# Performance work log

Measured on AMD Instinct MI355X. Metric: run time of the kernel, lower is better.

## Reference

```python
import jax, jax.numpy as jnp
import numpy as np

WS = 32          # window_size (== k passed to rounding helper)
R = 4            # num_relations
H = 8            # num_heads
D = 64           # out_features (head dim)
FIN = 256        # in_features
LENGTHS = [251, 247, 263, 255, 240, 258, 249, 260, 252, 245, 256, 250, 248, 261, 244, 254]


def _statics(lengths, ws):
    """Static index bookkeeping mirroring round_up_to_nearest_k_and_a_window_size,
    insert_zero_rows and the post-hoc index removal in forward()."""
    l = np.asarray(lengths, dtype=np.int64)
    tgt = (l + ws - 1) // ws * ws + ws            # per-graph padded length (+1 extra window)
    starts = np.concatenate([[0], np.cumsum(tgt)[:-1]])
    pad_even = starts - np.arange(len(l)) * ws + l  # padding start in trimmed frame
    pad_odd_win = (starts + tgt - ws) // ws         # window index of each extra padding window
    L = int(tgt.sum())
    w = L // ws
    # positions of real nodes inside the padded sequence
    pos = np.concatenate([s + np.arange(n) for s, n in zip(starts, l)])
    extra = set(pad_odd_win.tolist())
    rem_windows = np.array([i for i in range(w) if i not in extra], dtype=np.int64)
    Wp = len(rem_windows)
    removed = set()
    for p in pad_even:
        nm = (int(p) + ws - 1) // ws * ws
        removed.update(range(int(p), nm))
    rem_final = np.array([i for i in range(Wp * ws) if i not in removed], dtype=np.int64)
    return L, w, pos, rem_windows, rem_final


def setup_inputs() -> dict:
    key = jax.random.key(0)
    k1, k2, k3, k4, k5 = jax.random.split(key, 5)
    N = int(sum(LENGTHS))
    node_features = jax.random.normal(k1, (R, N, FIN), dtype=jnp.float32)
    Wq = jax.random.normal(k2, (H * D, FIN), dtype=jnp.float32) * 0.02
    b_q = jax.random.normal(k3, (H * D,), dtype=jnp.float32) * 0.02
    Wk = jax.random.normal(k4, (H * D, FIN), dtype=jnp.float32) * 0.02
    b_k = jax.random.normal(k5, (H * D,), dtype=jnp.float32) * 0.02
    num_nodes = jnp.asarray(LENGTHS, dtype=jnp.int64)
    return {"node_features": node_features, "Wq": Wq, "b_q": b_q, "Wk": Wk, "b_k": b_k,
            "num_nodes": num_nodes}


def reference(node_features, Wq, b_q, Wk, b_k, num_nodes):
    lengths = np.asarray(num_nodes).tolist()
    L, w, pos, rem_w, rem_f = _statics(lengths, WS)
    Rr, N, Fi = node_features.shape

    # insert_zero_rows: scatter real nodes into padded [R, L, F]; bool key mask [L]
    padded = jnp.zeros((Rr, L, Fi), node_features.dtype).at[:, pos].set(node_features)
    maskL = np.zeros(L, dtype=bool)
    maskL[pos] = True

    # Q/K projections -> [R*H, L, D]
    Q = (padded @ Wq.T + b_q).reshape(Rr, L, H, D).transpose(0, 2, 1, 3).reshape(Rr * H, L, D)
    K = (padded @ Wk.T + b_k).reshape(Rr, L, H, D).transpose(0, 2, 1, 3).reshape(Rr * H, L, D)

    scale = D ** -0.5
    qb = Q.reshape(-1, w, WS, D) * scale            # [B, w, ws, D]
    kb = K.reshape(-1, w, WS, D)
    # look_around keys (backward=1, forward=1, pad_value=-1)
    pk = jnp.pad(kb, ((0, 0), (1, 1), (0, 0), (0, 0)), constant_values=-1.0)
    k3 = jnp.concatenate([pk[:, i:i + w] for i in range(3)], axis=2)  # [B, w, 3ws, D]

    # static validity mask: key-position pad mask AND look-around of real-node mask
    t = np.arange(L).reshape(w, WS)
    pt = np.pad(t, ((1, 1), (0, 0)), constant_values=-1)
    t3 = np.concatenate([pt[i:i + w] for i in range(3)], axis=1)      # [w, 3ws]
    mw = maskL.reshape(w, WS)
    pm = np.pad(mw, ((1, 1), (0, 0)), constant_values=False)
    m3 = np.concatenate([pm[i:i + w] for i in range(3)], axis=1)      # [w, 3ws]
    valid = jnp.asarray(m3 & (t3 != -1))[None, :, None, :]            # [1, w, 1, 3ws]

    sim = jnp.einsum('bwid,bwjd->bwij', qb, k3)                        # [B, w, ws, 3ws]
    NEG = -jnp.finfo(sim.dtype).max
    sim = jnp.where(valid, sim, NEG)

    # drop pure-padding extra windows, softmax (dropout omitted: eval mode)
    attn = jax.nn.softmax(sim[:, rem_w], axis=-1)                      # [B, Wp, ws, 3ws]
    Wp = rem_w.shape[0]
    score = attn.reshape(Rr, H, Wp, WS, 3 * WS).mean(axis=1)           # [R, Wp, ws, 3ws]

    # displace blocks to banded rectangle, then trim first/last window of columns
    wi = np.arange(Wp)[:, None, None]
    ri = np.arange(WS)[None, :, None]
    ci = (np.arange(Wp) * WS)[:, None, None] + np.arange(3 * WS)[None, None, :]
    full = jnp.zeros((Rr, Wp, WS, (Wp + 2) * WS), score.dtype)
    full = full.at[:, wi, ri, ci].set(score)
    rect = full.reshape(Rr, Wp * WS, (Wp + 2) * WS)[:, :, WS:-WS]      # [R, Wp*ws, Wp*ws]

    # remove intra-window padding rows and columns
    rect = rect[:, rem_f][:, :, rem_f]                                 # [R, N, N]
    n = rem_f.shape[0]
    return rect.transpose(1, 0, 2).reshape(n, Rr * n)                  # [N, R*N]
```

## Files before the change

kernel.cpp:

```cpp
#include <hip/hip_runtime.h>
#include <stdint.h>

typedef float f32x4 __attribute__((ext_vector_type(4)));
typedef short s16x8 __attribute__((ext_vector_type(8)));
typedef unsigned short u16x4 __attribute__((ext_vector_type(4)));
typedef unsigned short u16x8 __attribute__((ext_vector_type(8)));

#define NG 16
__constant__ int c_LEN[NG]   = {251,247,263,255,240,258,249,260,252,245,256,250,248,261,244,254};
__constant__ int c_CUM[NG+1] = {0,251,498,761,1016,1256,1514,1763,2023,2275,2520,2776,3026,3274,3535,3779,4033};
__constant__ int c_KWC[NG+1] = {0,8,16,25,33,41,50,58,67,75,83,91,99,107,116,124,132};

#define NTOT 4033
#define RN   16132
#define NWIN 132
#define NEGF (-3.0e38f)

#define OUT_F32 65060356L
#define OUT_N4  16265089L
#define ZBLOCKS 2024
#define PBLOCKS 4048

#define OFF_WB 8259584
#define OFF_QK 8783872

__device__ __forceinline__ unsigned short f2bf(float f){
  union { float f; uint32_t u; } x; x.f = f;
  uint32_t u = x.u;
  u += 0x7fffu + ((u >> 16) & 1u);
  return (unsigned short)(u >> 16);
}

__device__ __forceinline__ f32x4 mfma16(s16x8 a, s16x8 b, f32x4 c){
  return __builtin_amdgcn_mfma_f32_16x16x32_bf16(a, b, c, 0, 0, 0);
}

#define NX4  1032448
#define NWQ4 32768
#define NCV4 1097984
__global__ void convert_kernel(const float* __restrict__ X,
                               const float* __restrict__ Wq,
                               const float* __restrict__ Wk,
                               unsigned short* __restrict__ Xb,
                               unsigned short* __restrict__ Wb){
  int i = blockIdx.x * 256 + threadIdx.x;
  if (i >= NCV4) return;
  const float* src; unsigned short* dst;
  if (i < NX4){ src = X + (size_t)i * 4; dst = Xb + (size_t)i * 4; }
  else {
    int k = i - NX4;
    if (k < NWQ4){ src = Wq + (size_t)k * 4; dst = Wb + (size_t)k * 4; }
    else         { src = Wk + (size_t)(k - NWQ4) * 4; dst = Wb + (size_t)k * 4; }
  }
  f32x4 v = *(const f32x4*)src;
  u16x4 o;
  #pragma unroll
  for (int c = 0; c < 4; ++c) o[c] = f2bf(v[c]);
  *(u16x4*)dst = o;
}

#define LP 68
__global__ __launch_bounds__(256) void projzero_kernel(const unsigned short* __restrict__ Xb,
                                                       const unsigned short* __restrict__ Wb,
                                                       const float* __restrict__ bq,
                                                       const float* __restrict__ bk,
                                                       unsigned short* __restrict__ QK,
                                                       float* __restrict__ out){
  __shared__ float tile[64 * LP];

  int bid = blockIdx.x;
  int grp = bid / 3;
  int rem = bid - grp * 3;

  if (rem == 2){
    f32x4 z = {0.f, 0.f, 0.f, 0.f};
    f32x4* o4 = (f32x4*)out;
    long stride = (long)ZBLOCKS * 256;
    for (long i = (long)grp * 256 + threadIdx.x; i < OUT_N4; i += stride)
      o4[i] = z;
    return;
  }

  int pi = grp * 2 + rem;
  int col0 = (pi & 15) * 64;
  int row0 = (pi >> 4) * 64;

  int tid  = threadIdx.x;
  int lane = tid & 63, wid = tid >> 6;
  int l15  = lane & 15, quad = lane >> 4;
  int wm = wid & 1, wn = wid >> 1;
  int rowW = row0 + wm * 32;
  int colW = col0 + wn * 32;

  f32x4 acc[2][2];
  #pragma unroll
  for (int m = 0; m < 2; ++m)
    #pragma unroll
    for (int n = 0; n < 2; ++n){ acc[m][n][0]=0.f; acc[m][n][1]=0.f; acc[m][n][2]=0.f; acc[m][n][3]=0.f; }

  int r0 = min(rowW + l15,      RN - 1);
  int r1 = min(rowW + 16 + l15, RN - 1);
  const unsigned short* a0p = Xb + (size_t)r0 * 256 + quad * 8;
  const unsigned short* a1p = Xb + (size_t)r1 * 256 + quad * 8;
  const unsigned short* b0p = Wb + (size_t)(colW + l15)      * 256 + quad * 8;
  const unsigned short* b1p = Wb + (size_t)(colW + 16 + l15) * 256 + quad * 8;

  #pragma unroll
  for (int k = 0; k < 256; k += 32){
    s16x8 a0 = *(const s16x8*)(a0p + k);
    s16x8 a1 = *(const s16x8*)(a1p + k);
    s16x8 b0 = *(const s16x8*)(b0p + k);
    s16x8 b1 = *(const s16x8*)(b1p + k);
    acc[0][0] = mfma16(a0, b0, acc[0][0]);
    acc[0][1] = mfma16(a0, b1, acc[0][1]);
    acc[1][0] = mfma16(a1, b0, acc[1][0]);
    acc[1][1] = mfma16(a1, b1, acc[1][1]);
  }

  #pragma unroll
  for (int m = 0; m < 2; ++m)
  #pragma unroll
  for (int n = 0; n < 2; ++n)
  #pragma unroll
  for (int g = 0; g < 4; ++g){
    int rL = wm * 32 + m * 16 + quad * 4 + g;
    int cL = wn * 32 + n * 16 + l15;
    tile[rL * LP + cL] = acc[m][n][g];
  }
  __syncthreads();

  int rL = tid >> 2;
  int cB = (tid & 3) * 16;
  int row = row0 + rL;
  if (row < RN){
    int col = col0 + cB;
    const float* bias = (col < 512) ? (bq + col) : (bk + col - 512);
    float sc = (col < 512) ? 0.125f : 1.0f;
    u16x8 o0, o1;
    #pragma unroll
    for (int i = 0; i < 8; ++i)
      o0[i] = f2bf((tile[rL * LP + cB + i] + bias[i]) * sc);
    #pragma unroll
    for (int i = 0; i < 8; ++i)
      o1[i] = f2bf((tile[rL * LP + cB + 8 + i] + bias[8 + i]) * sc);
    *(u16x8*)(QK + (size_t)row * 1024 + col)     = o0;
    *(u16x8*)(QK + (size_t)row * 1024 + col + 8) = o1;
  }
}

__global__ __launch_bounds__(512) void attn_kernel(const unsigned short* __restrict__ QK,
                                                   float* __restrict__ out){
  __shared__ float part[4][32 * 97];

  int b  = blockIdx.x;
  int r  = b / NWIN;
  int wq = b % NWIN;
  int g = 0;
  #pragma unroll
  for (int i = 0; i < NG; ++i) if (wq >= c_KWC[i + 1]) g = i + 1;
  int lw   = wq - c_KWC[g];
  int l    = c_LEN[g];
  int base = c_CUM[g];
  int qbeg = lw * 32;
  int qnum = min(32, l - qbeg);
  int kbeg = max(0, qbeg - 32);
  int kend = min(l, qbeg + 64);
  int knum = kend - kbeg;

  int tid  = threadIdx.x;
  int lane = tid & 63, wid = tid >> 6;
  int l15  = lane & 15, quad = lane >> 4;
  int rbase = r * NTOT + base;
  int h = wid;

  bool valid[6];
  #pragma unroll
  for (int n = 0; n < 6; ++n) valid[n] = (n * 16 + l15) < knum;

  s16x8 qf[2][2];
  #pragma unroll
  for (int m = 0; m < 2; ++m){
    int qi = min(qbeg + m * 16 + l15, l - 1);
    const unsigned short* qp = QK + (size_t)(rbase + qi) * 1024 + h * 64 + quad * 8;
    qf[m][0] = *(const s16x8*)qp;
    qf[m][1] = *(const s16x8*)(qp + 32);
  }
  f32x4 s[2][6];
  #pragma unroll
  for (int n = 0; n < 6; ++n){
    int ki = min(kbeg + n * 16 + l15, l - 1);
    const unsigned short* kp = QK + (size_t)(rbase + ki) * 1024 + 512 + h * 64 + quad * 8;
    s16x8 kf0 = *(const s16x8*)kp;
    s16x8 kf1 = *(const s16x8*)(kp + 32);
    #pragma unroll
    for (int m = 0; m < 2; ++m){
      f32x4 z; z[0]=0.f; z[1]=0.f; z[2]=0.f; z[3]=0.f;
      z = mfma16(qf[m][0], kf0, z);
      s[m][n] = mfma16(qf[m][1], kf1, z);
    }
  }
  #pragma unroll
  for (int m = 0; m < 2; ++m)
    #pragma unroll
    for (int n = 0; n < 6; ++n)
      if (!valid[n]){ s[m][n][0]=NEGF; s[m][n][1]=NEGF; s[m][n][2]=NEGF; s[m][n][3]=NEGF; }

  f32x4 accv[2][6];
  #pragma unroll
  for (int m = 0; m < 2; ++m){
    f32x4 mx = s[m][0];
    #pragma unroll
    for (int n = 1; n < 6; ++n)
      #pragma unroll
      for (int c = 0; c < 4; ++c) mx[c] = fmaxf(mx[c], s[m][n][c]);
    #pragma unroll
    for (int c = 0; c < 4; ++c){
      float v = mx[c];
      v = fmaxf(v, __shfl_xor(v, 1));
      v = fmaxf(v, __shfl_xor(v, 2));
      v = fmaxf(v, __shfl_xor(v, 4));
      v = fmaxf(v, __shfl_xor(v, 8));
      mx[c] = v;
    }
    f32x4 sum; sum[0]=0.f; sum[1]=0.f; sum[2]=0.f; sum[3]=0.f;
    #pragma unroll
    for (int n = 0; n < 6; ++n)
      #pragma unroll
      for (int c = 0; c < 4; ++c){
        float e = __expf(s[m][n][c] - mx[c]);
        s[m][n][c] = e;
        sum[c] += e;
      }
    #pragma unroll
    for (int c = 0; c < 4; ++c){
      float v = sum[c];
      v += __shfl_xor(v, 1);
      v += __shfl_xor(v, 2);
      v += __shfl_xor(v, 4);
      v += __shfl_xor(v, 8);
      sum[c] = v;
    }
    f32x4 scv;
    #pragma unroll
    for (int c = 0; c < 4; ++c) scv[c] = 0.125f / sum[c];
    #pragma unroll
    for (int n = 0; n < 6; ++n)
      #pragma unroll
      for (int c = 0; c < 4; ++c) accv[m][n][c] = s[m][n][c] * scv[c];
  }

  if (wid >= 4){
    #pragma unroll
    for (int m = 0; m < 2; ++m)
    #pragma unroll
    for (int n = 0; n < 6; ++n)
    #pragma unroll
    for (int c = 0; c < 4; ++c){
      int row = m * 16 + quad * 4 + c;
      int col = n * 16 + l15;
      part[wid - 4][row * 97 + col] = accv[m][n][c];
    }
  }
  __syncthreads();
  if (wid < 4){
    #pragma unroll
    for (int m = 0; m < 2; ++m)
    #pragma unroll
    for (int n = 0; n < 6; ++n)
    #pragma unroll
    for (int c = 0; c < 4; ++c){
      int row = m * 16 + quad * 4 + c;
      int col = n * 16 + l15;
      part[wid][row * 97 + col] += accv[m][n][c];
    }
  }
  __syncthreads();

  for (int e = tid; e < 32 * 96; e += 512){
    int row = e / 96, col = e % 96;
    if (row < qnum && col < knum){
      float v = part[0][row * 97 + col] + part[1][row * 97 + col]
              + part[2][row * 97 + col] + part[3][row * 97 + col];
      long nq = base + qbeg + row;
      long mk = base + kbeg + col;
      out[nq * (long)RN + (long)r * NTOT + mk] = v;
    }
  }
}

extern "C" void kernel_launch(void* const* d_in, const int* in_sizes, int n_in,
                              void* d_out, int out_size, void* d_ws, size_t ws_size,
                              hipStream_t stream){
  const float* X  = (const float*)d_in[0];
  const float* Wq = (const float*)d_in[1];
  const float* bq = (const float*)d_in[2];
  const float* Wk = (const float*)d_in[3];
  const float* bk = (const float*)d_in[4];
  float* out = (float*)d_out;

  char* ws = (char*)d_ws;
  unsigned short* Xb = (unsigned short*)ws;
  unsigned short* Wb = (unsigned short*)(ws + OFF_WB);
  unsigned short* QK = (unsigned short*)(ws + OFF_QK);

  convert_kernel<<<(NCV4 + 255) / 256, 256, 0, stream>>>(X, Wq, Wk, Xb, Wb);
  projzero_kernel<<<3 * ZBLOCKS, 256, 0, stream>>>(Xb, Wb, bq, bk, QK, out);
  attn_kernel<<<4 * NWIN, 512, 0, stream>>>(QK, out);
}
```

Baseline: 347.8 us.

## Split output zero-fill between projection and attention kernels, skipping band regions

The projection kernel now zero-fills only the first 2304 output rows. The attention kernel gains interleaved zero-fill blocks that clear the remaining rows while skipping the banded columns the attention blocks write. This moves part of the large memset so it overlaps attention compute and avoids writing the same band twice. The launch bound also allows 4 blocks per CU, and the softmax result is scaled in place. Correctness now depends on the zero-fill and band writes staying disjoint, and partial vectors fall back to scalar stores.

```diff
diff --git a/kernel.cpp b/kernel.cpp
--- a/kernel.cpp
+++ b/kernel.cpp
@@ -16,10 +16,10 @@
 #define NWIN 132
 #define NEGF (-3.0e38f)
 
-#define OUT_F32 65060356L
-#define OUT_N4  16265089L
+#define ZS 2304
+#define ZCHUNKA 9292032L
 #define ZBLOCKS 2024
-#define PBLOCKS 4048
+#define AZB 264
 
 #define OFF_WB 8259584
 #define OFF_QK 8783872
@@ -76,7 +76,7 @@
     f32x4 z = {0.f, 0.f, 0.f, 0.f};
     f32x4* o4 = (f32x4*)out;
     long stride = (long)ZBLOCKS * 256;
-    for (long i = (long)grp * 256 + threadIdx.x; i < OUT_N4; i += stride)
+    for (long i = (long)grp * 256 + threadIdx.x; i < ZCHUNKA; i += stride)
       o4[i] = z;
     return;
   }
@@ -148,11 +148,57 @@
   }
 }
 
-__global__ __launch_bounds__(512) void attn_kernel(const unsigned short* __restrict__ QK,
-                                                   float* __restrict__ out){
+__global__ __launch_bounds__(512, 4) void attnzero_kernel(const unsigned short* __restrict__ QK,
+                                                          float* __restrict__ out){
   __shared__ float part[4][32 * 97];
 
-  int b  = blockIdx.x;
+  int bid = blockIdx.x;
+  int grp = bid / 3;
+  int rem = bid - grp * 3;
+
+  if (rem == 2){
+    for (int row = ZS + grp; row < NTOT; row += AZB){
+      int g = 0;
+      #pragma unroll
+      for (int i = 0; i < NG; ++i) if (row >= c_CUM[i + 1]) g = i + 1;
+      int base = c_CUM[g], l = c_LEN[g];
+      int lw = (row - base) >> 5;
+      int kb = base + max(0, (lw << 5) - 32);
+      int ke = base + min(l, (lw << 5) + 64);
+      float* orow = out + (size_t)row * RN;
+      for (int c = threadIdx.x; c < 4033; c += 512){
+        int col0 = c << 2;
+        int r0 = (col0 >= 12099) ? 3 : (col0 >= 8066) ? 2 : (col0 >= 4033) ? 1 : 0;
+        int col3 = col0 + 3;
+        int r3 = (col3 >= 12099) ? 3 : (col3 >= 8066) ? 2 : (col3 >= 4033) ? 1 : 0;
+        if (r0 == r3){
+          int cr = col0 - r0 * NTOT;
+          if (cr + 4 <= kb || cr >= ke){
+            f32x4 z = {0.f, 0.f, 0.f, 0.f};
+            *(f32x4*)(orow + col0) = z;
+          } else if (cr >= kb && cr + 4 <= ke){
+          } else {
+            #pragma unroll
+            for (int i = 0; i < 4; ++i){
+              int cc = cr + i;
+              if (cc < kb || cc >= ke) orow[col0 + i] = 0.f;
+            }
+          }
+        } else {
+          #pragma unroll
+          for (int i = 0; i < 4; ++i){
+            int col = col0 + i;
+            int r = (col >= 12099) ? 3 : (col >= 8066) ? 2 : (col >= 4033) ? 1 : 0;
+            int cr = col - r * NTOT;
+            if (cr < kb || cr >= ke) orow[col] = 0.f;
+          }
+        }
+      }
+    }
+    return;
+  }
+
+  int b  = grp * 2 + rem;
   int r  = b / NWIN;
   int wq = b % NWIN;
   int g = 0;
@@ -205,7 +251,6 @@
     for (int n = 0; n < 6; ++n)
       if (!valid[n]){ s[m][n][0]=NEGF; s[m][n][1]=NEGF; s[m][n][2]=NEGF; s[m][n][3]=NEGF; }
 
-  f32x4 accv[2][6];
   #pragma unroll
   for (int m = 0; m < 2; ++m){
     f32x4 mx = s[m][0];
@@ -246,7 +291,7 @@
     #pragma unroll
     for (int n = 0; n < 6; ++n)
       #pragma unroll
-      for (int c = 0; c < 4; ++c) accv[m][n][c] = s[m][n][c] * scv[c];
+      for (int c = 0; c < 4; ++c) s[m][n][c] *= scv[c];
   }
 
   if (wid >= 4){
@@ -258,7 +303,7 @@
     for (int c = 0; c < 4; ++c){
       int row = m * 16 + quad * 4 + c;
       int col = n * 16 + l15;
-      part[wid - 4][row * 97 + col] = accv[m][n][c];
+      part[wid - 4][row * 97 + col] = s[m][n][c];
     }
   }
   __syncthreads();
@@ -271,7 +316,7 @@
     for (int c = 0; c < 4; ++c){
       int row = m * 16 + quad * 4 + c;
       int col = n * 16 + l15;
-      part[wid][row * 97 + col] += accv[m][n][c];
+      part[wid][row * 97 + col] += s[m][n][c];
     }
   }
   __syncthreads();
@@ -305,5 +350,5 @@
 
   convert_kernel<<<(NCV4 + 255) / 256, 256, 0, stream>>>(X, Wq, Wk, Xb, Wb);
   projzero_kernel<<<3 * ZBLOCKS, 256, 0, stream>>>(Xb, Wb, bq, bk, QK, out);
-  attn_kernel<<<4 * NWIN, 512, 0, stream>>>(QK, out);
-}
+  attnzero_kernel<<<3 * AZB, 512, 0, stream>>>(QK, out);
+}
```

New measurement: 357.2 us. 1.03x slower.

## Fuse fp32-to-bf16 conversion into projection GEMM and use nontemporal zero stores

Applied to the files above, without the earlier changes.

Removes the separate convert kernel and has the projection kernel load fp32 X, Wq and Wk directly, converting to bf16 in registers before the MFMA. This drops one launch and the round trip of writing and rereading the bf16 copies. In exchange each block now reads twice the bytes and redoes the conversion, because the weight tiles are reread by many blocks. The output zero-fill switches to nontemporal stores to reduce cache pollution, and a small register reuse in the attention softmax replaces the separate accv array.

```diff
diff --git a/kernel.cpp b/kernel.cpp
--- a/kernel.cpp
+++ b/kernel.cpp
@@ -3,7 +3,6 @@
 
 typedef float f32x4 __attribute__((ext_vector_type(4)));
 typedef short s16x8 __attribute__((ext_vector_type(8)));
-typedef unsigned short u16x4 __attribute__((ext_vector_type(4)));
 typedef unsigned short u16x8 __attribute__((ext_vector_type(8)));
 
 #define NG 16
@@ -16,13 +15,9 @@
 #define NWIN 132
 #define NEGF (-3.0e38f)
 
-#define OUT_F32 65060356L
 #define OUT_N4  16265089L
 #define ZBLOCKS 2024
-#define PBLOCKS 4048
-
-#define OFF_WB 8259584
-#define OFF_QK 8783872
+
 
 __device__ __forceinline__ unsigned short f2bf(float f){
   union { float f; uint32_t u; } x; x.f = f;
@@ -31,37 +26,24 @@
   return (unsigned short)(u >> 16);
 }
 
+__device__ __forceinline__ s16x8 cvt8(f32x4 lo, f32x4 hi){
+  s16x8 r;
+  #pragma unroll
+  for (int i = 0; i < 4; ++i){
+    r[i]     = (short)f2bf(lo[i]);
+    r[4 + i] = (short)f2bf(hi[i]);
+  }
+  return r;
+}
+
 __device__ __forceinline__ f32x4 mfma16(s16x8 a, s16x8 b, f32x4 c){
   return __builtin_amdgcn_mfma_f32_16x16x32_bf16(a, b, c, 0, 0, 0);
 }
 
-#define NX4  1032448
-#define NWQ4 32768
-#define NCV4 1097984
-__global__ void convert_kernel(const float* __restrict__ X,
-                               const float* __restrict__ Wq,
-                               const float* __restrict__ Wk,
-                               unsigned short* __restrict__ Xb,
-                               unsigned short* __restrict__ Wb){
-  int i = blockIdx.x * 256 + threadIdx.x;
-  if (i >= NCV4) return;
-  const float* src; unsigned short* dst;
-  if (i < NX4){ src = X + (size_t)i * 4; dst = Xb + (size_t)i * 4; }
-  else {
-    int k = i - NX4;
-    if (k < NWQ4){ src = Wq + (size_t)k * 4; dst = Wb + (size_t)k * 4; }
-    else         { src = Wk + (size_t)(k - NWQ4) * 4; dst = Wb + (size_t)k * 4; }
-  }
-  f32x4 v = *(const f32x4*)src;
-  u16x4 o;
-  #pragma unroll
-  for (int c = 0; c < 4; ++c) o[c] = f2bf(v[c]);
-  *(u16x4*)dst = o;
-}
-
 #define LP 68
-__global__ __launch_bounds__(256) void projzero_kernel(const unsigned short* __restrict__ Xb,
-                                                       const unsigned short* __restrict__ Wb,
+__global__ __launch_bounds__(256) void projzero_kernel(const float* __restrict__ X,
+                                                       const float* __restrict__ Wq,
+                                                       const float* __restrict__ Wk,
                                                        const float* __restrict__ bq,
                                                        const float* __restrict__ bk,
                                                        unsigned short* __restrict__ QK,
@@ -77,7 +59,7 @@
     f32x4* o4 = (f32x4*)out;
     long stride = (long)ZBLOCKS * 256;
     for (long i = (long)grp * 256 + threadIdx.x; i < OUT_N4; i += stride)
-      o4[i] = z;
+      __builtin_nontemporal_store(z, o4 + i);
     return;
   }
 
@@ -100,17 +82,21 @@
 
   int r0 = min(rowW + l15,      RN - 1);
   int r1 = min(rowW + 16 + l15, RN - 1);
-  const unsigned short* a0p = Xb + (size_t)r0 * 256 + quad * 8;
-  const unsigned short* a1p = Xb + (size_t)r1 * 256 + quad * 8;
-  const unsigned short* b0p = Wb + (size_t)(colW + l15)      * 256 + quad * 8;
-  const unsigned short* b1p = Wb + (size_t)(colW + 16 + l15) * 256 + quad * 8;
-
-  #pragma unroll
+  const float* a0p = X + (size_t)r0 * 256 + quad * 8;
+  const float* a1p = X + (size_t)r1 * 256 + quad * 8;
+  int c0 = colW + l15;
+  int c1 = colW + 16 + l15;
+  const float* b0p = (c0 < 512 ? Wq + (size_t)c0 * 256
+                               : Wk + (size_t)(c0 - 512) * 256) + quad * 8;
+  const float* b1p = (c1 < 512 ? Wq + (size_t)c1 * 256
+                               : Wk + (size_t)(c1 - 512) * 256) + quad * 8;
+
+  #pragma unroll 2
   for (int k = 0; k < 256; k += 32){
-    s16x8 a0 = *(const s16x8*)(a0p + k);
-    s16x8 a1 = *(const s16x8*)(a1p + k);
-    s16x8 b0 = *(const s16x8*)(b0p + k);
-    s16x8 b1 = *(const s16x8*)(b1p + k);
+    s16x8 a0 = cvt8(*(const f32x4*)(a0p + k), *(const f32x4*)(a0p + k + 4));
+    s16x8 a1 = cvt8(*(const f32x4*)(a1p + k), *(const f32x4*)(a1p + k + 4));
+    s16x8 b0 = cvt8(*(const f32x4*)(b0p + k), *(const f32x4*)(b0p + k + 4));
+    s16x8 b1 = cvt8(*(const f32x4*)(b1p + k), *(const f32x4*)(b1p + k + 4));
     acc[0][0] = mfma16(a0, b0, acc[0][0]);
     acc[0][1] = mfma16(a0, b1, acc[0][1]);
     acc[1][0] = mfma16(a1, b0, acc[1][0]);
@@ -205,7 +191,6 @@
     for (int n = 0; n < 6; ++n)
       if (!valid[n]){ s[m][n][0]=NEGF; s[m][n][1]=NEGF; s[m][n][2]=NEGF; s[m][n][3]=NEGF; }
 
-  f32x4 accv[2][6];
   #pragma unroll
   for (int m = 0; m < 2; ++m){
     f32x4 mx = s[m][0];
@@ -246,7 +231,7 @@
     #pragma unroll
     for (int n = 0; n < 6; ++n)
       #pragma unroll
-      for (int c = 0; c < 4; ++c) accv[m][n][c] = s[m][n][c] * scv[c];
+      for (int c = 0; c < 4; ++c) s[m][n][c] *= scv[c];
   }
 
   if (wid >= 4){
@@ -258,7 +243,7 @@
     for (int c = 0; c < 4; ++c){
       int row = m * 16 + quad * 4 + c;
       int col = n * 16 + l15;
-      part[wid - 4][row * 97 + col] = accv[m][n][c];
+      part[wid - 4][row * 97 + col] = s[m][n][c];
     }
   }
   __syncthreads();
@@ -271,7 +256,7 @@
     for (int c = 0; c < 4; ++c){
       int row = m * 16 + quad * 4 + c;
       int col = n * 16 + l15;
-      part[wid][row * 97 + col] += accv[m][n][c];
+      part[wid][row * 97 + col] += s[m][n][c];
     }
   }
   __syncthreads();
@@ -298,12 +283,8 @@
   const float* bk = (const float*)d_in[4];
   float* out = (float*)d_out;
 
-  char* ws = (char*)d_ws;
-  unsigned short* Xb = (unsigned short*)ws;
-  unsigned short* Wb = (unsigned short*)(ws + OFF_WB);
-  unsigned short* QK = (unsigned short*)(ws + OFF_QK);
-
-  convert_kernel<<<(NCV4 + 255) / 256, 256, 0, stream>>>(X, Wq, Wk, Xb, Wb);
-  projzero_kernel<<<3 * ZBLOCKS, 256, 0, stream>>>(Xb, Wb, bq, bk, QK, out);
+  unsigned short* QK = (unsigned short*)d_ws;
+
+  projzero_kernel<<<3 * ZBLOCKS, 256, 0, stream>>>(X, Wq, Wk, bq, bk, QK, out);
   attn_kernel<<<4 * NWIN, 512, 0, stream>>>(QK, out);
 }
```

Result: slower. 394.1 us (+13.3%).
